# Kernel tuning notes

Measured on AMD Instinct MI355X. Metric: run time of the kernel, lower is better.

The kernel has to match this reference:

```python
import jax, jax.numpy as jnp
import numpy as np

LAYER_START = 4
WS = 2  # context_window_size
EPS = 1e-8


def _alpha_for_k(tf, idx):
    # tf: [L, D] per-token layer features; idx: static window row indices (last entry is k)
    Wm = tf[idx]                       # [w, D]
    w = Wm.shape[0]
    _, R = jnp.linalg.qr(Wm.T)         # reduced QR of [D, w] -> R: [w, w]
    r = R[:, -1]
    sub = R[:-1, :-1]
    coln = jnp.linalg.norm(sub, axis=0)
    align = jnp.mean(sub / coln, axis=1) @ R[:-1, -1] / jnp.linalg.norm(r[:-1])
    align = 1.0 / (align * w * 2)
    nov = jnp.abs(r[-1]) / jnp.linalg.norm(r)
    return align, nov


def _unify_token(tf):
    # tf: [L, D] -> pooled [D]
    L = tf.shape[0]
    aligns, novs = [], []
    for k in range(L):  # loop over small fixed layer count (structurally distinct windows)
        # NOTE: original torch code token_feature[k-ws:k] yields an EMPTY slice for k < ws
        left = list(range(k - WS, k)) if k >= WS else []
        right = list(range(k + 1, min(k + WS + 1, L)))
        idx = np.array(left + right + [k], dtype=np.int32)
        a, n = _alpha_for_k(tf, idx)
        aligns.append(a)
        novs.append(n)
    aa = jnp.stack(aligns)
    nv = jnp.stack(novs)
    aa = aa / aa.sum()
    nv = nv / nv.sum()
    alpha = aa + nv
    alpha = alpha / alpha.sum()
    return tf.T @ alpha


def _token_var(tf):
    # tf: [L, D] -> variance (unbiased) of subdiagonal of cosine-sim map
    w = jnp.linalg.norm(tf, axis=1, keepdims=True)
    sim = (tf @ tf.T) / jnp.clip(w * w.T, EPS)
    return jnp.var(jnp.diagonal(sim, -1), ddof=1)


def reference(all_hidden_states, attention_mask):
    # all_hidden_states: [B, num_layers, S, D]; attention_mask: [B, S] (all sentences equal length)
    T = int(np.asarray(attention_mask).sum(axis=1)[0]) - 1  # unmask_num = sum(mask) - 1
    sf = all_hidden_states[:, LAYER_START:, :T, :]          # [B, L, T, D]
    per_tok = jax.vmap(jax.vmap(_unify_token, in_axes=1))(sf)  # [B, T, D]

    def per_sentence(s, ose):
        v = jax.vmap(_token_var, in_axes=1)(s)  # [T]
        v = v / v.sum()
        return ose.T @ v                        # [D]

    return jax.vmap(per_sentence)(sf, per_tok)  # [B, D]


def setup_inputs():
    key = jax.random.key(0)
    all_hidden_states = jax.random.normal(key, (8, 12, 512, 768), dtype=jnp.float32)
    attention_mask = jnp.ones((8, 512), dtype=jnp.int32)
    return {"all_hidden_states": all_hidden_states, "attention_mask": attention_mask}
```

## Files before the change

### kernel.cpp

```cpp
#include <hip/hip_runtime.h>
#include <math.h>

#define NLAYER_TOT 12
#define LAYER0 4
#define SMAX 512
#define DIM 768
#define NSEG 64

__host__ __device__ constexpr int gp(int i, int j) {
    return (i <= j) ? (i * 8 - i * (i - 1) / 2 + (j - i))
                    : (j * 8 - j * (j - 1) / 2 + (i - j));
}

__device__ inline float frcp(float x) { return __builtin_amdgcn_rcpf(x); }
__device__ inline float frsq(float x) { return __builtin_amdgcn_rsqf(x); }

__global__ void k_init(const int* __restrict__ mask, int* __restrict__ wsT) {
    __shared__ int red[512];
    int tid = threadIdx.x;
    red[tid] = mask[tid];
    __syncthreads();
    for (int s = 256; s >= 1; s >>= 1) {
        if (tid < s) red[tid] += red[tid + s];
        __syncthreads();
    }
    if (tid == 0) wsT[0] = red[0] - 1;
}

template <int W>
__device__ inline void alpha_nov(const float (&A)[36], const int (&idx)[5],
                                 float& align_o, float& nov_o) {
    float Gs[W][W];
#pragma unroll
    for (int i = 0; i < W; ++i)
#pragma unroll
        for (int j = i; j < W; ++j) {
            float v = A[gp(idx[i], idx[j])];
            Gs[i][j] = v;
            Gs[j][i] = v;
        }
    float R[W][W];
#pragma unroll
    for (int j = 0; j < W; ++j) {
#pragma unroll
        for (int i = 0; i <= j; ++i) {
            float s = Gs[i][j];
#pragma unroll
            for (int q = 0; q < i; ++q) s -= R[q][i] * R[q][j];
            if (i == j) R[i][j] = s * frsq(s);
            else        R[i][j] = s * frcp(R[i][i]);
        }
    }
    float ic[W - 1];
#pragma unroll
    for (int j = 0; j < W - 1; ++j) ic[j] = frsq(Gs[j][j]);
    float m[W - 1];
#pragma unroll
    for (int i = 0; i < W - 1; ++i) {
        float s = 0.0f;
#pragma unroll
        for (int j = i; j < W - 1; ++j) s += R[i][j] * ic[j];
        m[i] = s * (1.0f / (float)(W - 1));
    }
    float num = 0.0f, n1 = 0.0f;
#pragma unroll
    for (int i = 0; i < W - 1; ++i) {
        num += m[i] * R[i][W - 1];
        n1 += R[i][W - 1] * R[i][W - 1];
    }
    float align_raw = num * frsq(n1);
    align_o = frcp(align_raw * (float)W * 2.0f);
    nov_o = fabsf(R[W - 1][W - 1]) * frsq(Gs[W - 1][W - 1]);
}

__global__ __launch_bounds__(256, 2) void k_main(const float* __restrict__ in,
                                                 const int* __restrict__ wsT,
                                                 float* __restrict__ P,
                                                 float* __restrict__ Vp) {
    int T = wsT[0];
    int seg = blockIdx.x;
    int b = blockIdx.y;
    int wave = threadIdx.x >> 6;
    int lane = threadIdx.x & 63;

    __shared__ float part[DIM];
    __shared__ float vpart;
    for (int i = threadIdx.x; i < DIM; i += 256) part[i] = 0.0f;
    if (threadIdx.x == 0) vpart = 0.0f;
    __syncthreads();

    const float* bbase = in + (size_t)(b * NLAYER_TOT + LAYER0) * SMAX * DIM;

    float4 acc12[3];
#pragma unroll
    for (int it = 0; it < 3; ++it) acc12[it] = make_float4(0.f, 0.f, 0.f, 0.f);
    float vloc = 0.0f;

    static constexpr int IDX0[5] = {1, 2, 0, 0, 0};
    static constexpr int IDX1[5] = {2, 3, 1, 0, 0};
    static constexpr int IDX2[5] = {0, 1, 3, 4, 2};
    static constexpr int IDX3[5] = {1, 2, 4, 5, 3};
    static constexpr int IDX4[5] = {2, 3, 5, 6, 4};
    static constexpr int IDX5[5] = {3, 4, 6, 7, 5};
    static constexpr int IDX6[5] = {4, 5, 7, 6, 0};
    static constexpr int IDX7[5] = {5, 6, 7, 0, 0};

#pragma unroll
    for (int ti = 0; ti < 2; ++ti) {
        int t = seg * 8 + wave * 2 + ti;
        if (t >= T) continue;
        const float* base = bbase + (size_t)t * DIM;
        float4 x[8][3];
#pragma unroll
        for (int k = 0; k < 8; ++k)
#pragma unroll
            for (int it = 0; it < 3; ++it)
                x[k][it] = *(const float4*)(base + (size_t)k * SMAX * DIM + it * 256 + lane * 4);
        float g[36];
#pragma unroll
        for (int p = 0; p < 36; ++p) g[p] = 0.0f;
#pragma unroll
        for (int it = 0; it < 3; ++it) {
            int p = 0;
#pragma unroll
            for (int i = 0; i < 8; ++i)
#pragma unroll
                for (int j = i; j < 8; ++j) {
                    g[p] += x[i][it].x * x[j][it].x + x[i][it].y * x[j][it].y +
                            x[i][it].z * x[j][it].z + x[i][it].w * x[j][it].w;
                    ++p;
                }
        }
#pragma unroll
        for (int p = 0; p < 36; ++p) {
#pragma unroll
            for (int off = 32; off >= 1; off >>= 1) g[p] += __shfl_xor(g[p], off, 64);
        }
        float a[8], n[8];
        alpha_nov<3>(g, IDX0, a[0], n[0]);
        alpha_nov<3>(g, IDX1, a[1], n[1]);
        alpha_nov<5>(g, IDX2, a[2], n[2]);
        alpha_nov<5>(g, IDX3, a[3], n[3]);
        alpha_nov<5>(g, IDX4, a[4], n[4]);
        alpha_nov<5>(g, IDX5, a[5], n[5]);
        alpha_nov<4>(g, IDX6, a[6], n[6]);
        alpha_nov<3>(g, IDX7, a[7], n[7]);
        float sa = 0.0f, sn = 0.0f;
#pragma unroll
        for (int k = 0; k < 8; ++k) { sa += a[k]; sn += n[k]; }
        float isa = frcp(sa), isn = frcp(sn);
        float al[8], ss = 0.0f;
#pragma unroll
        for (int k = 0; k < 8; ++k) { al[k] = a[k] * isa + n[k] * isn; ss += al[k]; }
        float iss = frcp(ss);
        float c[7], mu = 0.0f;
#pragma unroll
        for (int i = 0; i < 7; ++i) {
            float denom = g[gp(i, i)] * g[gp(i + 1, i + 1)];
            c[i] = g[gp(i, i + 1)] * frsq(denom > 1e-16f ? denom : 1e-16f);
            mu += c[i];
        }
        mu *= (1.0f / 7.0f);
        float var = 0.0f;
#pragma unroll
        for (int i = 0; i < 7; ++i) var += (c[i] - mu) * (c[i] - mu);
        float vraw = var * (1.0f / 6.0f);
        vloc += vraw;
        float p8[8];
#pragma unroll
        for (int k = 0; k < 8; ++k) p8[k] = al[k] * iss * vraw;
#pragma unroll
        for (int it = 0; it < 3; ++it) {
#pragma unroll
            for (int k = 0; k < 8; ++k) {
                acc12[it].x += p8[k] * x[k][it].x;
                acc12[it].y += p8[k] * x[k][it].y;
                acc12[it].z += p8[k] * x[k][it].z;
                acc12[it].w += p8[k] * x[k][it].w;
            }
        }
    }

#pragma unroll
    for (int it = 0; it < 3; ++it) {
        int d = it * 256 + lane * 4;
        atomicAdd(&part[d + 0], acc12[it].x);
        atomicAdd(&part[d + 1], acc12[it].y);
        atomicAdd(&part[d + 2], acc12[it].z);
        atomicAdd(&part[d + 3], acc12[it].w);
    }
    if (lane == 0) atomicAdd(&vpart, vloc);
    __syncthreads();

    float* pd = P + ((size_t)b * NSEG + seg) * DIM;
    for (int i = threadIdx.x; i < DIM; i += 256) pd[i] = part[i];
    if (threadIdx.x == 0) Vp[b * NSEG + seg] = vpart;
}

__global__ void k_reduce(const float* __restrict__ P, const float* __restrict__ Vp,
                         float* __restrict__ out) {
    int b = blockIdx.x;
    int d = threadIdx.x;
    __shared__ float vred[64];
    __shared__ float vinv;
    if (d < 64) vred[d] = Vp[b * NSEG + d];
    __syncthreads();
    if (d == 0) {
        float s = 0.0f;
        for (int i = 0; i < 64; ++i) s += vred[i];
        vinv = 1.0f / s;
    }
    __syncthreads();
    float s = 0.0f;
    const float* pb = P + (size_t)b * NSEG * DIM;
    for (int seg = 0; seg < NSEG; ++seg) s += pb[(size_t)seg * DIM + d];
    out[b * DIM + d] = s * vinv;
}

extern "C" void kernel_launch(void* const* d_in, const int* in_sizes, int n_in,
                              void* d_out, int out_size, void* d_ws, size_t ws_size,
                              hipStream_t stream) {
    const float* hs = (const float*)d_in[0];
    const int* mask = (const int*)d_in[1];
    float* out = (float*)d_out;
    char* ws = (char*)d_ws;
    int* wsT = (int*)ws;
    float* P = (float*)(ws + 256);
    float* Vp = (float*)(ws + 256 + (size_t)8 * NSEG * DIM * 4);

    k_init<<<1, 512, 0, stream>>>(mask, wsT);
    k_main<<<dim3(NSEG, 8), 256, 0, stream>>>(hs, wsT, P, Vp);
    k_reduce<<<8, DIM, 0, stream>>>(P, Vp, out);
}
```

Before: 232.9 us.

## Cut register pressure by streaming chunks and re-reading inputs, one token per wave

Each wave now handles one token instead of two, and the block count doubles. Rather than keeping all 24 float4 values live, the kernel streams the three 256-wide chunks with a one-chunk prefetch. It then reloads the inputs from memory (likely an L2 hit) for the weighted-sum pass. The Gram reduction uses DPP row shifts plus two xor shuffles in place of six shuffles. The aim is fewer VGPRs and higher occupancy, paid for with a second global read of every token and a larger partial buffer for k_reduce to sum.

```diff
diff --git a/kernel.cpp b/kernel.cpp
--- a/kernel.cpp
+++ b/kernel.cpp
@@ -5,7 +5,7 @@
 #define LAYER0 4
 #define SMAX 512
 #define DIM 768
-#define NSEG 64
+#define NSEG 128
 
 __host__ __device__ constexpr int gp(int i, int j) {
     return (i <= j) ? (i * 8 - i * (i - 1) / 2 + (j - i))
@@ -14,6 +14,16 @@
 
 __device__ inline float frcp(float x) { return __builtin_amdgcn_rcpf(x); }
 __device__ inline float frsq(float x) { return __builtin_amdgcn_rsqf(x); }
+
+__device__ inline float wave_reduce_add(float v) {
+    v += __int_as_float(__builtin_amdgcn_update_dpp(0, __float_as_int(v), 0x121, 0xF, 0xF, true));
+    v += __int_as_float(__builtin_amdgcn_update_dpp(0, __float_as_int(v), 0x122, 0xF, 0xF, true));
+    v += __int_as_float(__builtin_amdgcn_update_dpp(0, __float_as_int(v), 0x124, 0xF, 0xF, true));
+    v += __int_as_float(__builtin_amdgcn_update_dpp(0, __float_as_int(v), 0x128, 0xF, 0xF, true));
+    v += __shfl_xor(v, 16, 64);
+    v += __shfl_xor(v, 32, 64);
+    return v;
+}
 
 __global__ void k_init(const int* __restrict__ mask, int* __restrict__ wsT) {
     __shared__ int red[512];
@@ -89,53 +99,59 @@
     if (threadIdx.x == 0) vpart = 0.0f;
     __syncthreads();
 
-    const float* bbase = in + (size_t)(b * NLAYER_TOT + LAYER0) * SMAX * DIM;
-
+    int t = seg * 4 + wave;
     float4 acc12[3];
 #pragma unroll
     for (int it = 0; it < 3; ++it) acc12[it] = make_float4(0.f, 0.f, 0.f, 0.f);
     float vloc = 0.0f;
 
-    static constexpr int IDX0[5] = {1, 2, 0, 0, 0};
-    static constexpr int IDX1[5] = {2, 3, 1, 0, 0};
-    static constexpr int IDX2[5] = {0, 1, 3, 4, 2};
-    static constexpr int IDX3[5] = {1, 2, 4, 5, 3};
-    static constexpr int IDX4[5] = {2, 3, 5, 6, 4};
-    static constexpr int IDX5[5] = {3, 4, 6, 7, 5};
-    static constexpr int IDX6[5] = {4, 5, 7, 6, 0};
-    static constexpr int IDX7[5] = {5, 6, 7, 0, 0};
-
-#pragma unroll
-    for (int ti = 0; ti < 2; ++ti) {
-        int t = seg * 8 + wave * 2 + ti;
-        if (t >= T) continue;
-        const float* base = bbase + (size_t)t * DIM;
-        float4 x[8][3];
+    if (t < T) {
+        const float* base = in + ((size_t)(b * NLAYER_TOT + LAYER0) * SMAX + t) * DIM;
+
+        float g[36];
+#pragma unroll
+        for (int p = 0; p < 36; ++p) g[p] = 0.0f;
+        float4 cur[8], nxt[8];
 #pragma unroll
         for (int k = 0; k < 8; ++k)
-#pragma unroll
-            for (int it = 0; it < 3; ++it)
-                x[k][it] = *(const float4*)(base + (size_t)k * SMAX * DIM + it * 256 + lane * 4);
-        float g[36];
-#pragma unroll
-        for (int p = 0; p < 36; ++p) g[p] = 0.0f;
+            cur[k] = *(const float4*)(base + (size_t)k * SMAX * DIM + lane * 4);
 #pragma unroll
         for (int it = 0; it < 3; ++it) {
+            if (it < 2) {
+                int d = (it + 1) * 256 + lane * 4;
+#pragma unroll
+                for (int k = 0; k < 8; ++k)
+                    nxt[k] = *(const float4*)(base + (size_t)k * SMAX * DIM + d);
+            }
             int p = 0;
 #pragma unroll
             for (int i = 0; i < 8; ++i)
 #pragma unroll
                 for (int j = i; j < 8; ++j) {
-                    g[p] += x[i][it].x * x[j][it].x + x[i][it].y * x[j][it].y +
-                            x[i][it].z * x[j][it].z + x[i][it].w * x[j][it].w;
+                    g[p] += cur[i].x * cur[j].x + cur[i].y * cur[j].y +
+                            cur[i].z * cur[j].z + cur[i].w * cur[j].w;
                     ++p;
                 }
-        }
-#pragma unroll
-        for (int p = 0; p < 36; ++p) {
-#pragma unroll
-            for (int off = 32; off >= 1; off >>= 1) g[p] += __shfl_xor(g[p], off, 64);
-        }
+            if (it < 2) {
+#pragma unroll
+                for (int k = 0; k < 8; ++k) cur[k] = nxt[k];
+            }
+        }
+#pragma unroll
+        for (int p = 0; p < 36; ++p) g[p] = wave_reduce_add(g[p]);
+
+#pragma unroll
+        for (int k = 0; k < 8; ++k)
+            cur[k] = *(const float4*)(base + (size_t)k * SMAX * DIM + lane * 4);
+
+        static constexpr int IDX0[5] = {1, 2, 0, 0, 0};
+        static constexpr int IDX1[5] = {2, 3, 1, 0, 0};
+        static constexpr int IDX2[5] = {0, 1, 3, 4, 2};
+        static constexpr int IDX3[5] = {1, 2, 4, 5, 3};
+        static constexpr int IDX4[5] = {2, 3, 5, 6, 4};
+        static constexpr int IDX5[5] = {3, 4, 6, 7, 5};
+        static constexpr int IDX6[5] = {4, 5, 7, 6, 0};
+        static constexpr int IDX7[5] = {5, 6, 7, 0, 0};
         float a[8], n[8];
         alpha_nov<3>(g, IDX0, a[0], n[0]);
         alpha_nov<3>(g, IDX1, a[1], n[1]);
@@ -165,31 +181,42 @@
 #pragma unroll
         for (int i = 0; i < 7; ++i) var += (c[i] - mu) * (c[i] - mu);
         float vraw = var * (1.0f / 6.0f);
-        vloc += vraw;
+        vloc = vraw;
         float p8[8];
 #pragma unroll
         for (int k = 0; k < 8; ++k) p8[k] = al[k] * iss * vraw;
+
 #pragma unroll
         for (int it = 0; it < 3; ++it) {
+            if (it < 2) {
+                int d = (it + 1) * 256 + lane * 4;
+#pragma unroll
+                for (int k = 0; k < 8; ++k)
+                    nxt[k] = *(const float4*)(base + (size_t)k * SMAX * DIM + d);
+            }
 #pragma unroll
             for (int k = 0; k < 8; ++k) {
-                acc12[it].x += p8[k] * x[k][it].x;
-                acc12[it].y += p8[k] * x[k][it].y;
-                acc12[it].z += p8[k] * x[k][it].z;
-                acc12[it].w += p8[k] * x[k][it].w;
-            }
-        }
-    }
-
-#pragma unroll
-    for (int it = 0; it < 3; ++it) {
-        int d = it * 256 + lane * 4;
-        atomicAdd(&part[d + 0], acc12[it].x);
-        atomicAdd(&part[d + 1], acc12[it].y);
-        atomicAdd(&part[d + 2], acc12[it].z);
-        atomicAdd(&part[d + 3], acc12[it].w);
-    }
-    if (lane == 0) atomicAdd(&vpart, vloc);
+                acc12[it].x += p8[k] * cur[k].x;
+                acc12[it].y += p8[k] * cur[k].y;
+                acc12[it].z += p8[k] * cur[k].z;
+                acc12[it].w += p8[k] * cur[k].w;
+            }
+            if (it < 2) {
+#pragma unroll
+                for (int k = 0; k < 8; ++k) cur[k] = nxt[k];
+            }
+        }
+
+#pragma unroll
+        for (int it = 0; it < 3; ++it) {
+            int d = it * 256 + lane * 4;
+            atomicAdd(&part[d + 0], acc12[it].x);
+            atomicAdd(&part[d + 1], acc12[it].y);
+            atomicAdd(&part[d + 2], acc12[it].z);
+            atomicAdd(&part[d + 3], acc12[it].w);
+        }
+        if (lane == 0) atomicAdd(&vpart, vloc);
+    }
     __syncthreads();
 
     float* pd = P + ((size_t)b * NSEG + seg) * DIM;
@@ -201,13 +228,13 @@
                          float* __restrict__ out) {
     int b = blockIdx.x;
     int d = threadIdx.x;
-    __shared__ float vred[64];
+    __shared__ float vred[NSEG];
     __shared__ float vinv;
-    if (d < 64) vred[d] = Vp[b * NSEG + d];
+    if (d < NSEG) vred[d] = Vp[b * NSEG + d];
     __syncthreads();
     if (d == 0) {
         float s = 0.0f;
-        for (int i = 0; i < 64; ++i) s += vred[i];
+        for (int i = 0; i < NSEG; ++i) s += vred[i];
         vinv = 1.0f / s;
     }
     __syncthreads();
```

New measurement: 224.1 us. 1.04x faster.
